# Kernel optimization log

Measured on AMD Instinct MI355X. Metric: run time of the kernel, lower is better.

The kernel has to match this reference:

```python
import jax, jax.numpy as jnp
import numpy as np

DIM = 2048
K = 8                 # top_k
M = 16                # max_transients
BIND_FRAC = 0.15
BETA = 0.05
GAMMA = 0.9
LIFETIME = 5
B, T = 64, 256

_iu, _ju = np.triu_indices(K, k=1)   # row-major: matches torch's (ii outer, jj inner) loop order
IU = jnp.asarray(_iu, jnp.int32)
JU = jnp.asarray(_ju, jnp.int32)


def _renorm(s):
    n = jnp.sqrt(jnp.sum(jnp.abs(s) ** 2, axis=-1, keepdims=True))
    return s / jnp.maximum(n, 1e-8)


def setup_inputs() -> dict:
    key = jax.random.key(0)
    ks = jax.random.split(key, 5)
    return {
        "x": jax.random.normal(ks[0], (B, T, DIM), jnp.float32),
        "tape_re": jax.random.normal(ks[1], (DIM,), jnp.float32) / np.sqrt(DIM).astype(np.float32),
        "tape_im": jax.random.normal(ks[2], (DIM,), jnp.float32) / np.sqrt(DIM).astype(np.float32),
        "eta_param": jnp.asarray(0.1, jnp.float32),
        "torque_bias_re": jax.random.normal(ks[3], (DIM,), jnp.float32) * 0.01,
        "torque_bias_im": jax.random.normal(ks[4], (DIM,), jnp.float32) * 0.01,
    }


def _per_batch(h, s, ti, tj, mre, mim, cnt, eta, tbias):
    """One timestep for one batch element. s: [D] complex64, transients: 5 arrays of [M]."""
    c = h * s                               # Hadamard reception
    _, top_idx = jax.lax.top_k(jnp.abs(c), K)
    top_c = c[top_idx]
    tm = jnp.abs(top_c)
    ph = jnp.angle(top_c)
    # co-resonance scores for the K*(K-1)/2 pairs; torch detaches via .item()
    score = jax.lax.stop_gradient(tm[IU] * tm[JU] * jnp.cos(ph[IU] - ph[JU]))
    pos = score > 0
    n_pos = jnp.sum(pos.astype(jnp.int32))
    n_bind = jnp.maximum(1, (n_pos.astype(jnp.float32) * BIND_FRAC).astype(jnp.int32))
    sorted_desc = -jnp.sort(-jnp.where(pos, score, -jnp.inf))
    theta_idx = jnp.minimum(n_bind - 1, jnp.maximum(n_pos - 1, 0))
    theta = sorted_desc[theta_idx]
    bind = (score >= theta) & (n_pos > 0)   # theta>0 so only positive scores pass

    ci = top_idx[IU]
    cj = top_idx[JU]
    prod = s[ci] * s[cj]
    mnew = jax.lax.stop_gradient(BETA * prod / jnp.maximum(jnp.abs(prod), 1e-8))  # torch detaches via .item()

    def step(tr, inp):
        ti, tj, mre, mim, cnt = tr
        ci_p, cj_p, do, mr, mi = inp
        active = cnt > 0
        match = active & (((ti == ci_p) & (tj == cj_p)) | ((ti == cj_p) & (tj == ci_p)))
        has_match = jnp.any(match)
        midx = jnp.argmax(match)
        free = ~active
        has_free = jnp.any(free)
        fidx = jnp.argmax(free)
        refresh = do & has_match
        insert = do & (~has_match) & has_free
        cnt = jnp.where(refresh, cnt.at[midx].set(LIFETIME), cnt)
        ti = jnp.where(insert, ti.at[fidx].set(ci_p), ti)
        tj = jnp.where(insert, tj.at[fidx].set(cj_p), tj)
        mre = jnp.where(insert, mre.at[fidx].set(mr), mre)
        mim = jnp.where(insert, mim.at[fidx].set(mi), mim)
        cnt = jnp.where(insert, cnt.at[fidx].set(LIFETIME), cnt)
        return (ti, tj, mre, mim, cnt), None

    (ti, tj, mre, mim, cnt), _ = jax.lax.scan(
        step, (ti, tj, mre, mim, cnt), (ci, cj, bind, mnew.real, mnew.imag))

    # decay all transients
    mre = mre * GAMMA
    mim = mim * GAMMA
    cnt = cnt - 1
    alive = (cnt > 0) & (jnp.sqrt(mre * mre + mim * mim) > 1e-6)
    cnt = jnp.where(alive, cnt, 0)
    mre = jnp.where(alive, mre, 0.0)
    mim = jnp.where(alive, mim, 0.0)

    # augment state with transients (scatter-add to both endpoints)
    s_re = s.real.at[ti].add(0.1 * mre).at[tj].add(0.1 * mre)
    s_im = s.imag.at[ti].add(0.1 * mim).at[tj].add(0.1 * mim)
    s_aug = jax.lax.complex(s_re, s_im)

    c_aug = h * s_aug
    re_c = c_aug.real
    im_c = c_aug.imag
    res_mask = ((re_c > 1e-6) & (jnp.abs(im_c) < re_c)).astype(jnp.float32)
    tor_mask = ((re_c < -1e-6) | (jnp.abs(im_c) >= jnp.abs(re_c))).astype(jnp.float32)
    orth_mask = 1.0 - res_mask - tor_mask
    update = eta * (c_aug * (1.0 - orth_mask) + tor_mask * tbias)
    s_new = _renorm(s + update)
    return s_new, ti, tj, mre, mim, cnt


def _forward(x, tape_re, tape_im, eta_param, torque_bias_re, torque_bias_im):
    Bb, Tt, D = x.shape
    s0 = _renorm(jax.lax.complex(tape_re, tape_im)[None, :])
    s0 = jnp.broadcast_to(s0, (Bb, D))
    eta = jnp.abs(eta_param)
    tbias = jax.lax.complex(torque_bias_re, torque_bias_im)
    ti0 = jnp.zeros((Bb, M), jnp.int32)
    tj0 = jnp.zeros((Bb, M), jnp.int32)
    mre0 = jnp.zeros((Bb, M), jnp.float32)
    mim0 = jnp.zeros((Bb, M), jnp.float32)
    cnt0 = jnp.zeros((Bb, M), jnp.int32)

    step_b = jax.vmap(_per_batch, in_axes=(0, 0, 0, 0, 0, 0, 0, None, None))

    def time_step(carry, h_t):
        s, ti, tj, mre, mim, cnt = carry
        s, ti, tj, mre, mim, cnt = step_b(h_t, s, ti, tj, mre, mim, cnt, eta, tbias)
        return (s, ti, tj, mre, mim, cnt), jnp.abs(s)

    _, outs = jax.lax.scan(time_step, (s0, ti0, tj0, mre0, mim0, cnt0),
                           jnp.transpose(x, (1, 0, 2)))  # [T,B,D]
    return jnp.transpose(outs, (1, 0, 2))                # [B,T,D]


def reference(x, tape_re, tape_im, eta_param, torque_bias_re, torque_bias_im):
    return _forward(x, tape_re, tape_im, eta_param, torque_bias_re, torque_bias_im)
```

## Files before the change

kernel.cpp:

```cpp
#include <hip/hip_runtime.h>
#include <math.h>

#define DIM_ 2048
#define KTOP 8
#define MSLOT 16
#define TSTEPS 256
#define NB 64
#define NTHREADS 320
#define NWORK 256
#define EPT 8

static_assert(NWORK * EPT == DIM_, "mapping");

#define DPP0(src, ctrl, rm) __builtin_amdgcn_update_dpp(0, (src), (ctrl), (rm), 0xf, true)

__device__ __forceinline__ void ced(double &a, double &b) {
  double mx = fmax(a, b);
  b = fmin(a, b);
  a = mx;
}

__device__ __forceinline__ void sort8_desc(double k[8]) {
  ced(k[0],k[1]); ced(k[2],k[3]); ced(k[4],k[5]); ced(k[6],k[7]);
  ced(k[0],k[2]); ced(k[1],k[3]); ced(k[4],k[6]); ced(k[5],k[7]);
  ced(k[1],k[2]); ced(k[5],k[6]);
  ced(k[0],k[4]); ced(k[1],k[5]); ced(k[2],k[6]); ced(k[3],k[7]);
  ced(k[2],k[4]); ced(k[3],k[5]);
  ced(k[1],k[2]); ced(k[3],k[4]); ced(k[5],k[6]);
}

template <int CTRL, int RM>
__device__ __forceinline__ void merge_level(double k[8]) {
  double b[8];
#pragma unroll
  for (int i = 0; i < 8; i++) {
    int lo = DPP0(__double2loint(k[i]), CTRL, RM);
    int hi = DPP0(__double2hiint(k[i]), CTRL, RM);
    b[i] = __hiloint2double(hi, lo);
  }
#pragma unroll
  for (int i = 0; i < 8; i++) k[i] = fmax(k[i], b[7 - i]);
  ced(k[0],k[4]); ced(k[1],k[5]); ced(k[2],k[6]); ced(k[3],k[7]);
  ced(k[0],k[2]); ced(k[1],k[3]); ced(k[4],k[6]); ced(k[5],k[7]);
  ced(k[0],k[1]); ced(k[2],k[3]); ced(k[4],k[5]); ced(k[6],k[7]);
}

#define FMAX_STAGE(x, ctrl, rm)                                                \
  x = fmaxf(x, __int_as_float(DPP0(__float_as_int(x), ctrl, rm)))
#define FADD_STAGE(x, ctrl, rm)                                                \
  x = x + __int_as_float(DPP0(__float_as_int(x), ctrl, rm))

__device__ __forceinline__ float wave_max_f32(float x) {
  FMAX_STAGE(x, 0x111, 0xf);
  FMAX_STAGE(x, 0x112, 0xf);
  FMAX_STAGE(x, 0x114, 0xf);
  FMAX_STAGE(x, 0x118, 0xf);
  FMAX_STAGE(x, 0x142, 0xa);
  FMAX_STAGE(x, 0x143, 0xc);
  return x;
}
__device__ __forceinline__ float wave_sum_f32(float x) {
  FADD_STAGE(x, 0x111, 0xf);
  FADD_STAGE(x, 0x112, 0xf);
  FADD_STAGE(x, 0x114, 0xf);
  FADD_STAGE(x, 0x118, 0xf);
  FADD_STAGE(x, 0x142, 0xa);
  FADD_STAGE(x, 0x143, 0xc);
  return x;
}
__device__ __forceinline__ int rl63(int v) {
  return __builtin_amdgcn_readlane(v, 63);
}

__global__ void __launch_bounds__(NTHREADS)
me_fused(const float *__restrict__ x, const float *__restrict__ tape_re,
         const float *__restrict__ tape_im, const float *__restrict__ eta_param,
         const float *__restrict__ tbias_re, const float *__restrict__ tbias_im,
         float *__restrict__ out) {
  __shared__ float4 sc4[DIM_];
  __shared__ float2 dxy[DIM_];
  __shared__ unsigned long long cand_lds[4 * KTOP];
  __shared__ float red_sh[4];

  const int tid = threadIdx.x;
  const int lane = tid & 63;
  const int wid = tid >> 6;
  const int wtid = tid - 64;
  const int b = blockIdx.x;

  const float eta = fabsf(eta_param[0]);

  float vre[EPT], vim[EPT], tbre_[EPT], tbim_[EPT];
  float hcur[EPT], hnext[EPT];
  const float *xb = x + (size_t)b * TSTEPS * DIM_;

  if (wid > 0) {
    float acc = 0.f;
#pragma unroll
    for (int j = 0; j < EPT; j++) {
      int e = wtid + NWORK * j;
      float a = tape_re[e], c2 = tape_im[e];
      vre[j] = a; vim[j] = c2;
      tbre_[j] = tbias_re[e]; tbim_[j] = tbias_im[e];
      hcur[j] = xb[e]; hnext[j] = hcur[j];
      acc += a * a + c2 * c2;
    }
    float ws = wave_sum_f32(acc);
    if (lane == 63) red_sh[wid - 1] = ws;
  }

  int s_ti = 0, s_tj = 0, s_cnt = 0;
  float s_mre = 0.f, s_mim = 0.f;

  __syncthreads();

  for (int t = 0; t < TSTEPS; t++) {
    if (wid > 0) {
      double key[EPT];
#pragma unroll
      for (int j = 0; j < EPT; j++) {
        int e = wtid + NWORK * j;
        float h = hcur[j];
        float cr = h * vre[j], ci = h * vim[j];
        float av = sqrtf(cr * cr + ci * ci);
        key[j] = __hiloint2double(__float_as_int(av), ~e);
        sc4[e] = make_float4(h, vre[j], vim[j], 0.f);
        dxy[e] = make_float2(0.f, 0.f);
      }
      sort8_desc(key);
      merge_level<0x111, 0xf>(key);
      merge_level<0x112, 0xf>(key);
      merge_level<0x114, 0xf>(key);
      merge_level<0x118, 0xf>(key);
      merge_level<0x142, 0xa>(key);
      merge_level<0x143, 0xc>(key);
      if (lane == 63) {
#pragma unroll
        for (int r = 0; r < KTOP; r++)
          cand_lds[(wid - 1) * KTOP + r] =
              (unsigned long long)__double_as_longlong(key[r]);
      }
    }
    __syncthreads();

    float ivn;
    {
      float tot = red_sh[0] + red_sh[1] + red_sh[2] + red_sh[3];
      ivn = 1.f / fmaxf(sqrtf(tot), 1e-8f);
    }

    float osr[EPT], osi[EPT];

    if (wid == 0) {
      double c[8];
#pragma unroll
      for (int r = 0; r < KTOP; r++) {
        unsigned long long v = (lane < 4) ? cand_lds[lane * KTOP + r] : 0ull;
        c[r] = __longlong_as_double((long long)v);
      }
      merge_level<0x111, 0xf>(c);
      merge_level<0x112, 0xf>(c);
      int top[KTOP];
#pragma unroll
      for (int r = 0; r < KTOP; r++)
        top[r] = ~__builtin_amdgcn_readlane(__double2loint(c[r]), 3);

      int pi = (lane < 28) ? lane : 27;
      int ii = 0, base = 0;
      if (pi >= 7)  { ii = 1; base = 7;  }
      if (pi >= 13) { ii = 2; base = 13; }
      if (pi >= 18) { ii = 3; base = 18; }
      if (pi >= 22) { ii = 4; base = 22; }
      if (pi >= 25) { ii = 5; base = 25; }
      if (pi >= 27) { ii = 6; base = 27; }
      int jj = ii + 1 + (pi - base);
      int gi = top[0];
      if (ii == 1) gi = top[1];
      if (ii == 2) gi = top[2];
      if (ii == 3) gi = top[3];
      if (ii == 4) gi = top[4];
      if (ii == 5) gi = top[5];
      if (ii == 6) gi = top[6];
      int gj = top[1];
      if (jj == 2) gj = top[2];
      if (jj == 3) gj = top[3];
      if (jj == 4) gj = top[4];
      if (jj == 5) gj = top[5];
      if (jj == 6) gj = top[6];
      if (jj == 7) gj = top[7];

      float4 c4i = sc4[gi], c4j = sc4[gj];
      float sri = c4i.y * ivn, sii2 = c4i.z * ivn;
      float srj = c4j.y * ivn, sij = c4j.z * ivn;
      float cri = c4i.x * sri, cii = c4i.x * sii2;
      float crj = c4j.x * srj, cij = c4j.x * sij;
      float score = cri * crj + cii * cij;
      bool valid = (lane < 28);
      bool pos = valid && (score > 0.f);
      unsigned long long posmask = __ballot(pos);
      int npos = __popcll(posmask);
      float pr = sri * srj - sii2 * sij;
      float pq = sri * sij + sii2 * srj;
      float ap = fmaxf(sqrtf(pr * pr + pq * pq), 1e-8f);
      float mr = (0.05f * pr) / ap, mi = (0.05f * pq) / ap;

      unsigned long long bmask = 0ull;
      if (npos > 0) {
        int nbind = (int)((float)npos * 0.15f);
        if (nbind < 1) nbind = 1;
        float val = pos ? score : -__builtin_inff();
        float th = 0.f;
        for (int k2 = 0; k2 < nbind; ++k2) {
          float mx = wave_max_f32(val);
          th = __int_as_float(rl63(__float_as_int(mx)));
          if (k2 + 1 < nbind) {
            unsigned long long em = __ballot(val == th);
            if (lane == (int)__builtin_ctzll(em)) val = -__builtin_inff();
          }
        }
        bool bind = valid && (score >= th);
        bmask = __ballot(bind);
      }
      while (bmask) {
        int pp = (int)__builtin_ctzll(bmask);
        bmask &= bmask - 1;
        int pci = __builtin_amdgcn_readlane(gi, pp);
        int pcj = __builtin_amdgcn_readlane(gj, pp);
        int pmr = __builtin_amdgcn_readlane(__float_as_int(mr), pp);
        int pmi = __builtin_amdgcn_readlane(__float_as_int(mi), pp);
        bool isslot = (lane < MSLOT);
        bool match = isslot && (s_cnt > 0) &&
                     ((s_ti == pci && s_tj == pcj) ||
                      (s_ti == pcj && s_tj == pci));
        unsigned long long mm = __ballot(match);
        if (mm != 0ull) {
          if (lane == (int)__builtin_ctzll(mm)) s_cnt = 5;
        } else {
          unsigned long long fm = __ballot(isslot && s_cnt <= 0);
          if (fm != 0ull && lane == (int)__builtin_ctzll(fm)) {
            s_ti = pci; s_tj = pcj;
            s_mre = __int_as_float(pmr); s_mim = __int_as_float(pmi);
            s_cnt = 5;
          }
        }
      }
      if (lane < MSLOT) {
        s_mre *= 0.9f; s_mim *= 0.9f; s_cnt -= 1;
        bool alive = (s_cnt > 0) &&
                     (sqrtf(s_mre * s_mre + s_mim * s_mim) > 1e-6f);
        if (!alive) { s_cnt = 0; s_mre = 0.f; s_mim = 0.f; }
        atomicAdd(&dxy[s_ti].x, 0.1f * s_mre);
        atomicAdd(&dxy[s_tj].x, 0.1f * s_mre);
        atomicAdd(&dxy[s_ti].y, 0.1f * s_mim);
        atomicAdd(&dxy[s_tj].y, 0.1f * s_mim);
      }
    } else {
      if (t + 1 < TSTEPS) {
        const float *xr = xb + (size_t)(t + 1) * DIM_;
#pragma unroll
        for (int j = 0; j < EPT; j++) hnext[j] = xr[wtid + NWORK * j];
      }
      if (t > 0) {
        float *op = out + ((size_t)b * TSTEPS + (t - 1)) * DIM_;
#pragma unroll
        for (int j = 0; j < EPT; j++) {
          float sr = vre[j] * ivn, si = vim[j] * ivn;
          op[wtid + NWORK * j] = sqrtf(sr * sr + si * si);
        }
      }
#pragma unroll
      for (int j = 0; j < EPT; j++) {
        float sri = vre[j] * ivn, sii2 = vim[j] * ivn;
        osr[j] = sri; osi[j] = sii2;
        float h = hcur[j];
        float car = h * sri, cai = h * sii2;
        bool res = (car > 1e-6f) && (fabsf(cai) < car);
        bool tor = (car < -1e-6f) || (fabsf(cai) >= fabsf(car));
        float m1 = (res || tor) ? 1.f : 0.f;
        float mt = tor ? 1.f : 0.f;
        float ur = eta * (car * m1 + mt * tbre_[j]);
        float ui = eta * (cai * m1 + mt * tbim_[j]);
        vre[j] = sri + ur; vim[j] = sii2 + ui;
      }
    }
    __syncthreads();

    if (wid > 0) {
      float2 dd[EPT];
#pragma unroll
      for (int j = 0; j < EPT; j++) dd[j] = dxy[wtid + NWORK * j];
      float acc2 = 0.f;
#pragma unroll
      for (int j = 0; j < EPT; j++) {
        if (dd[j].x != 0.f || dd[j].y != 0.f) {
          float ar = osr[j] + dd[j].x, ai = osi[j] + dd[j].y;
          float h = hcur[j];
          float car = h * ar, cai = h * ai;
          bool res = (car > 1e-6f) && (fabsf(cai) < car);
          bool tor = (car < -1e-6f) || (fabsf(cai) >= fabsf(car));
          float m1 = (res || tor) ? 1.f : 0.f;
          float mt = tor ? 1.f : 0.f;
          float ur = eta * (car * m1 + mt * tbre_[j]);
          float ui = eta * (cai * m1 + mt * tbim_[j]);
          vre[j] = osr[j] + ur; vim[j] = osi[j] + ui;
        }
        acc2 += vre[j] * vre[j] + vim[j] * vim[j];
      }
      float ws = wave_sum_f32(acc2);
      if (lane == 63) red_sh[wid - 1] = ws;
#pragma unroll
      for (int j = 0; j < EPT; j++) hcur[j] = hnext[j];
    }
  }

  __syncthreads();
  if (wid > 0) {
    float tot = red_sh[0] + red_sh[1] + red_sh[2] + red_sh[3];
    float ivnF = 1.f / fmaxf(sqrtf(tot), 1e-8f);
    float *op = out + ((size_t)b * TSTEPS + (TSTEPS - 1)) * DIM_;
#pragma unroll
    for (int j = 0; j < EPT; j++) {
      float sr = vre[j] * ivnF, si = vim[j] * ivnF;
      op[wtid + NWORK * j] = sqrtf(sr * sr + si * si);
    }
  }
}

extern "C" void kernel_launch(void *const *d_in, const int *in_sizes, int n_in,
                              void *d_out, int out_size, void *d_ws,
                              size_t ws_size, hipStream_t stream) {
  const float *x = (const float *)d_in[0];
  const float *tre = (const float *)d_in[1];
  const float *tim = (const float *)d_in[2];
  const float *eta = (const float *)d_in[3];
  const float *tbre = (const float *)d_in[4];
  const float *tbim = (const float *)d_in[5];
  float *out = (float *)d_out;
  me_fused<<<NB, NTHREADS, 0, stream>>>(x, tre, tim, eta, tbre, tbim, out);
}
```

Before: 1.064 ms.

## Double worker waves to 8 with 4 elements per thread and lazy dxy clearing

Raises the block from 4 to 8 worker waves, halving per-thread elements. The per-thread sort shrinks to a 4-sort plus a half merge, and the leader wave gains one more merge level over 8 wave candidates. The dxy scratch buffer is no longer zeroed every step; it is zeroed once at start and then only at entries that were touched, and atomics are skipped for dead slots. This shortens the serial per-step critical path, at the cost of more waves to synchronize and an extra merge stage.

```diff
diff --git a/kernel.cpp b/kernel.cpp
--- a/kernel.cpp
+++ b/kernel.cpp
@@ -6,9 +6,9 @@
 #define MSLOT 16
 #define TSTEPS 256
 #define NB 64
-#define NTHREADS 320
-#define NWORK 256
-#define EPT 8
+#define NTHREADS 576
+#define NWORK 512
+#define EPT 4
 
 static_assert(NWORK * EPT == DIM_, "mapping");
 
@@ -20,13 +20,25 @@
   a = mx;
 }
 
-__device__ __forceinline__ void sort8_desc(double k[8]) {
+__device__ __forceinline__ void sort4_desc(double k[8]) {
+  ced(k[0],k[1]); ced(k[2],k[3]);
+  ced(k[0],k[2]); ced(k[1],k[3]);
+  ced(k[1],k[2]);
+}
+
+template <int CTRL, int RM>
+__device__ __forceinline__ void merge_first4(double k[8]) {
+  double b[4];
+#pragma unroll
+  for (int i = 0; i < 4; i++) {
+    int lo = DPP0(__double2loint(k[i]), CTRL, RM);
+    int hi = DPP0(__double2hiint(k[i]), CTRL, RM);
+    b[i] = __hiloint2double(hi, lo);
+  }
+  k[4] = b[3]; k[5] = b[2]; k[6] = b[1]; k[7] = b[0];
+  ced(k[0],k[4]); ced(k[1],k[5]); ced(k[2],k[6]); ced(k[3],k[7]);
+  ced(k[0],k[2]); ced(k[1],k[3]); ced(k[4],k[6]); ced(k[5],k[7]);
   ced(k[0],k[1]); ced(k[2],k[3]); ced(k[4],k[5]); ced(k[6],k[7]);
-  ced(k[0],k[2]); ced(k[1],k[3]); ced(k[4],k[6]); ced(k[5],k[7]);
-  ced(k[1],k[2]); ced(k[5],k[6]);
-  ced(k[0],k[4]); ced(k[1],k[5]); ced(k[2],k[6]); ced(k[3],k[7]);
-  ced(k[2],k[4]); ced(k[3],k[5]);
-  ced(k[1],k[2]); ced(k[3],k[4]); ced(k[5],k[6]);
 }
 
 template <int CTRL, int RM>
@@ -79,8 +91,8 @@
          float *__restrict__ out) {
   __shared__ float4 sc4[DIM_];
   __shared__ float2 dxy[DIM_];
-  __shared__ unsigned long long cand_lds[4 * KTOP];
-  __shared__ float red_sh[4];
+  __shared__ unsigned long long cand_lds[8 * KTOP];
+  __shared__ float red_sh[8];
 
   const int tid = threadIdx.x;
   const int lane = tid & 63;
@@ -103,6 +115,7 @@
       vre[j] = a; vim[j] = c2;
       tbre_[j] = tbias_re[e]; tbim_[j] = tbias_im[e];
       hcur[j] = xb[e]; hnext[j] = hcur[j];
+      dxy[e] = make_float2(0.f, 0.f);
       acc += a * a + c2 * c2;
     }
     float ws = wave_sum_f32(acc);
@@ -116,7 +129,7 @@
 
   for (int t = 0; t < TSTEPS; t++) {
     if (wid > 0) {
-      double key[EPT];
+      double key[8];
 #pragma unroll
       for (int j = 0; j < EPT; j++) {
         int e = wtid + NWORK * j;
@@ -125,10 +138,9 @@
         float av = sqrtf(cr * cr + ci * ci);
         key[j] = __hiloint2double(__float_as_int(av), ~e);
         sc4[e] = make_float4(h, vre[j], vim[j], 0.f);
-        dxy[e] = make_float2(0.f, 0.f);
-      }
-      sort8_desc(key);
-      merge_level<0x111, 0xf>(key);
+      }
+      sort4_desc(key);
+      merge_first4<0x111, 0xf>(key);
       merge_level<0x112, 0xf>(key);
       merge_level<0x114, 0xf>(key);
       merge_level<0x118, 0xf>(key);
@@ -145,7 +157,8 @@
 
     float ivn;
     {
-      float tot = red_sh[0] + red_sh[1] + red_sh[2] + red_sh[3];
+      float tot = (red_sh[0] + red_sh[1]) + (red_sh[2] + red_sh[3]) +
+                  (red_sh[4] + red_sh[5]) + (red_sh[6] + red_sh[7]);
       ivn = 1.f / fmaxf(sqrtf(tot), 1e-8f);
     }
 
@@ -155,15 +168,16 @@
       double c[8];
 #pragma unroll
       for (int r = 0; r < KTOP; r++) {
-        unsigned long long v = (lane < 4) ? cand_lds[lane * KTOP + r] : 0ull;
+        unsigned long long v = (lane < 8) ? cand_lds[lane * KTOP + r] : 0ull;
         c[r] = __longlong_as_double((long long)v);
       }
       merge_level<0x111, 0xf>(c);
       merge_level<0x112, 0xf>(c);
+      merge_level<0x114, 0xf>(c);
       int top[KTOP];
 #pragma unroll
       for (int r = 0; r < KTOP; r++)
-        top[r] = ~__builtin_amdgcn_readlane(__double2loint(c[r]), 3);
+        top[r] = ~__builtin_amdgcn_readlane(__double2loint(c[r]), 7);
 
       int pi = (lane < 28) ? lane : 27;
       int ii = 0, base = 0;
@@ -249,10 +263,12 @@
         bool alive = (s_cnt > 0) &&
                      (sqrtf(s_mre * s_mre + s_mim * s_mim) > 1e-6f);
         if (!alive) { s_cnt = 0; s_mre = 0.f; s_mim = 0.f; }
-        atomicAdd(&dxy[s_ti].x, 0.1f * s_mre);
-        atomicAdd(&dxy[s_tj].x, 0.1f * s_mre);
-        atomicAdd(&dxy[s_ti].y, 0.1f * s_mim);
-        atomicAdd(&dxy[s_tj].y, 0.1f * s_mim);
+        if (s_cnt > 0) {
+          atomicAdd(&dxy[s_ti].x, 0.1f * s_mre);
+          atomicAdd(&dxy[s_tj].x, 0.1f * s_mre);
+          atomicAdd(&dxy[s_ti].y, 0.1f * s_mim);
+          atomicAdd(&dxy[s_tj].y, 0.1f * s_mim);
+        }
       }
     } else {
       if (t + 1 < TSTEPS) {
@@ -293,6 +309,7 @@
 #pragma unroll
       for (int j = 0; j < EPT; j++) {
         if (dd[j].x != 0.f || dd[j].y != 0.f) {
+          dxy[wtid + NWORK * j] = make_float2(0.f, 0.f);
           float ar = osr[j] + dd[j].x, ai = osi[j] + dd[j].y;
           float h = hcur[j];
           float car = h * ar, cai = h * ai;
@@ -315,7 +332,8 @@
 
   __syncthreads();
   if (wid > 0) {
-    float tot = red_sh[0] + red_sh[1] + red_sh[2] + red_sh[3];
+    float tot = (red_sh[0] + red_sh[1]) + (red_sh[2] + red_sh[3]) +
+                (red_sh[4] + red_sh[5]) + (red_sh[6] + red_sh[7]);
     float ivnF = 1.f / fmaxf(sqrtf(tot), 1e-8f);
     float *op = out + ((size_t)b * TSTEPS + (TSTEPS - 1)) * DIM_;
 #pragma unroll
```

Result: no change. 1.081 ms (+1.7%).
